# Kernel optimization log

Measured on AMD Instinct MI355X. Metric: run time of the kernel, lower is better.

Reference implementation:

```python
import jax, jax.numpy as jnp
import numpy as np

N_NODES = 100000
N_EDGES = 1600000
IN_C, HID_C, OUT_C = 128, 128, 64


def setup_inputs() -> dict:
    key = jax.random.key(0)
    ks = jax.random.split(key, 8)
    x = jax.random.normal(ks[0], (N_NODES, IN_C), dtype=jnp.float32)
    edge_index = jax.random.randint(ks[1], (2, N_EDGES), 0, N_NODES, dtype=jnp.int32)
    def lin(k, fan_in, fan_out):
        # kaiming-uniform-ish init like torch Linear
        bound = 1.0 / np.sqrt(fan_in)
        return jax.random.uniform(k, (fan_in, fan_out), dtype=jnp.float32, minval=-bound, maxval=bound)
    W1_l = lin(ks[2], IN_C, HID_C)
    W1_r = lin(ks[3], IN_C, HID_C)
    b1 = jnp.zeros((HID_C,), jnp.float32)
    W2_l = lin(ks[4], HID_C, OUT_C)
    W2_r = lin(ks[5], HID_C, OUT_C)
    b2 = jnp.zeros((OUT_C,), jnp.float32)
    return {"x": x, "edge_index": edge_index,
            "W1_l": W1_l, "W1_r": W1_r, "b1": b1,
            "W2_l": W2_l, "W2_r": W2_r, "b2": b2}


def _sage_conv(x, src, dst, W_l, W_r, b, n_nodes):
    # mean-aggregate neighbor features: gather x[src], scatter-add to dst, / degree
    msgs = jnp.take(x, src, axis=0)                       # [E, F]
    agg = jax.ops.segment_sum(msgs, dst, num_segments=n_nodes)  # [N, F]
    deg = jax.ops.segment_sum(jnp.ones((src.shape[0],), x.dtype), dst,
                              num_segments=n_nodes)       # [N]
    agg = agg / jnp.maximum(deg, 1.0)[:, None]
    return agg @ W_l + x @ W_r + b


def reference(x, edge_index, W1_l, W1_r, b1, W2_l, W2_r, b2):
    src, dst = edge_index[0], edge_index[1]
    n = x.shape[0]
    h = _sage_conv(x, src, dst, W1_l, W1_r, b1, n)
    h = jax.nn.relu(h)
    # dropout is identity in eval/inference mode
    out = _sage_conv(h, src, dst, W2_l, W2_r, b2, n)
    return out
```

## Files before the change

kernel.cpp:

```cpp
#include <hip/hip_runtime.h>

constexpr int NNODES = 100000;
constexpr int NEDGES = 1600000;
constexpr int K = 128;
constexpr int NBUCKET = 391;
constexpr int BCAP = 6144;
constexpr int A_EPB = NEDGES / 256;

typedef __attribute__((ext_vector_type(8))) short bf16x8;
typedef __attribute__((ext_vector_type(4))) float f32x4;

__device__ __forceinline__ unsigned short f2bf(float f) {
    unsigned u = __float_as_uint(f);
    unsigned r = (u + 0x7fffu + ((u >> 16) & 1u)) >> 16;
    return (unsigned short)r;
}
__device__ __forceinline__ void acc2(float& a0, float& a1, unsigned u) {
    a0 += __uint_as_float(u << 16);
    a1 += __uint_as_float(u & 0xffff0000u);
}
__device__ __forceinline__ void acc8(float* a, uint4 v) {
    acc2(a[0], a[1], v.x); acc2(a[2], a[3], v.y);
    acc2(a[4], a[5], v.z); acc2(a[6], a[7], v.w);
}

__global__ void zero_int_kernel(int* __restrict__ p, int n) {
    int i = blockIdx.x * 256 + threadIdx.x;
    if (i < n) p[i] = 0;
}

__global__ void xcast_kernel(const float4* __restrict__ in, uint4* __restrict__ out, int n8) {
    int i = blockIdx.x * 256 + threadIdx.x;
    if (i >= n8) return;
    float4 a = in[2 * i], b = in[2 * i + 1];
    uint4 w;
    w.x = (unsigned)f2bf(a.x) | ((unsigned)f2bf(a.y) << 16);
    w.y = (unsigned)f2bf(a.z) | ((unsigned)f2bf(a.w) << 16);
    w.z = (unsigned)f2bf(b.x) | ((unsigned)f2bf(b.y) << 16);
    w.w = (unsigned)f2bf(b.z) | ((unsigned)f2bf(b.w) << 16);
    out[i] = w;
}

__global__ void wprep_kernel(const float* __restrict__ W1l, const float* __restrict__ W1r,
                             const float* __restrict__ W2l, const float* __restrict__ W2r,
                             unsigned short* __restrict__ Wt1l, unsigned short* __restrict__ Wt1r,
                             unsigned short* __restrict__ Wt2) {
    int idx = blockIdx.x * 256 + threadIdx.x;
    if (idx >= 128 * 128) return;
    int n = idx >> 7, k = idx & 127;
    Wt1l[idx] = f2bf(W1l[k * 128 + n]);
    Wt1r[idx] = f2bf(W1r[k * 128 + n]);
    Wt2[idx]  = f2bf(n < 64 ? W2l[k * 64 + n] : W2r[k * 64 + (n - 64)]);
}

__global__ __launch_bounds__(256) void binA_kernel(
    const int* __restrict__ src, const int* __restrict__ dst,
    int* __restrict__ bucket_alloc, int2* __restrict__ regions)
{
    __shared__ int hist[NBUCKET];
    __shared__ int lstart[NBUCKET];
    __shared__ int gbase[NBUCKET];
    __shared__ int cur[NBUCKET];
    __shared__ int sD[A_EPB];
    __shared__ int sS[A_EPB];
    __shared__ int oD[A_EPB];
    __shared__ int oS[A_EPB];
    const int tid = threadIdx.x;
    for (int i = tid; i < NBUCKET; i += 256) hist[i] = 0;
    __syncthreads();
    const int e0 = blockIdx.x * A_EPB;
    for (int i = tid; i < A_EPB; i += 256) {
        int d = dst[e0 + i];
        sD[i] = d; sS[i] = src[e0 + i];
        atomicAdd(&hist[d >> 8], 1);
    }
    __syncthreads();
    if (tid == 0) {
        int acc = 0;
        for (int b = 0; b < NBUCKET; ++b) { lstart[b] = acc; acc += hist[b]; }
    }
    __syncthreads();
    for (int b = tid; b < NBUCKET; b += 256) {
        gbase[b] = atomicAdd(&bucket_alloc[b], hist[b]);
        cur[b] = lstart[b];
    }
    __syncthreads();
    for (int i = tid; i < A_EPB; i += 256) {
        int d = sD[i];
        int p = atomicAdd(&cur[d >> 8], 1);
        oD[p] = d; oS[p] = sS[i];
    }
    __syncthreads();
    for (int j = tid; j < A_EPB; j += 256) {
        int d = oD[j];
        int b = d >> 8;
        int pos = gbase[b] + (j - lstart[b]);
        if (pos < BCAP)
            regions[(size_t)b * BCAP + pos] = make_int2(d, oS[j]);
    }
}

__global__ void scanB_kernel(const int* __restrict__ bucket_alloc, int* __restrict__ bucket_base) {
    __shared__ int tmp[512];
    int t = threadIdx.x;
    int v = (t < NBUCKET) ? min(bucket_alloc[t], BCAP) : 0;
    tmp[t] = v;
    __syncthreads();
    #pragma unroll
    for (int off = 1; off < 512; off <<= 1) {
        int u = (t >= off) ? tmp[t - off] : 0;
        __syncthreads();
        tmp[t] += u;
        __syncthreads();
    }
    if (t < NBUCKET) bucket_base[t] = tmp[t] - v;
}

__global__ __launch_bounds__(256) void binB_kernel(
    const int2* __restrict__ regions, const int* __restrict__ bucket_alloc,
    const int* __restrict__ bucket_base,
    int* __restrict__ row_start, int* __restrict__ row_end, int* __restrict__ csr_src)
{
    __shared__ int hist[256];
    __shared__ int loff[256];
    __shared__ int cur[256];
    __shared__ int sD[BCAP];
    __shared__ int sS[BCAP];
    __shared__ int sorted[BCAP];
    const int b = blockIdx.x;
    const int tid = threadIdx.x;
    const int n = min(bucket_alloc[b], BCAP);
    const int base = bucket_base[b];
    hist[tid] = 0;
    __syncthreads();
    for (int i = tid; i < n; i += 256) {
        int2 rec = regions[(size_t)b * BCAP + i];
        sD[i] = rec.x; sS[i] = rec.y;
        atomicAdd(&hist[rec.x & 255], 1);
    }
    __syncthreads();
    int v = hist[tid];
    loff[tid] = v;
    __syncthreads();
    #pragma unroll
    for (int off = 1; off < 256; off <<= 1) {
        int u = (tid >= off) ? loff[tid - off] : 0;
        __syncthreads();
        loff[tid] += u;
        __syncthreads();
    }
    int excl = loff[tid] - v;
    cur[tid] = excl;
    int node = b * 256 + tid;
    if (node < NNODES) {
        row_start[node] = base + excl;
        row_end[node] = base + excl + v;
    }
    __syncthreads();
    for (int i = tid; i < n; i += 256) {
        int p = atomicAdd(&cur[sD[i] & 255], 1);
        sorted[p] = sS[i];
    }
    __syncthreads();
    for (int j = tid; j < n; j += 256)
        csr_src[base + j] = sorted[j];
}

__device__ __forceinline__ int xcd_swizzle(int bid, int nwg) {
    int xcd = bid & 7;
    int idx = bid >> 3;
    int q = nwg >> 3, r = nwg & 7;
    int base = (xcd < r) ? xcd * (q + 1) : r * (q + 1) + (xcd - r) * q;
    return base + idx;
}

template<int F, bool ADDV, bool OUTBF>
__global__ void gather_mean_bf16_kernel(const int* __restrict__ row_start,
                                        const int* __restrict__ row_end,
                                        const int* __restrict__ csr_src,
                                        const unsigned short* __restrict__ feat,
                                        const float* __restrict__ add,
                                        void* __restrict__ outp, int nwg) {
    constexpr int G = F / 8;
    constexpr int NPB = 256 / G;
    int blk = xcd_swizzle(blockIdx.x, nwg);
    int node = blk * NPB + threadIdx.x / G;
    int lane = threadIdx.x % G;
    if (node >= NNODES) return;
    int beg = row_start[node];
    int end = row_end[node];
    const uint4* fp = reinterpret_cast<const uint4*>(feat);
    float a[8];
    #pragma unroll
    for (int q = 0; q < 8; ++q) a[q] = 0.f;
    int j = beg;
    for (; j + 3 < end; j += 4) {
        int s0 = csr_src[j];
        int s1 = csr_src[j + 1];
        int s2 = csr_src[j + 2];
        int s3 = csr_src[j + 3];
        uint4 v0 = fp[(size_t)s0 * G + lane];
        uint4 v1 = fp[(size_t)s1 * G + lane];
        uint4 v2 = fp[(size_t)s2 * G + lane];
        uint4 v3 = fp[(size_t)s3 * G + lane];
        acc8(a, v0); acc8(a, v1); acc8(a, v2); acc8(a, v3);
    }
    for (; j < end; ++j) {
        uint4 v0 = fp[(size_t)csr_src[j] * G + lane];
        acc8(a, v0);
    }
    float inv = 1.0f / fmaxf((float)(end - beg), 1.0f);
    #pragma unroll
    for (int q = 0; q < 8; ++q) a[q] *= inv;
    if (OUTBF) {
        uint4 w;
        w.x = (unsigned)f2bf(a[0]) | ((unsigned)f2bf(a[1]) << 16);
        w.y = (unsigned)f2bf(a[2]) | ((unsigned)f2bf(a[3]) << 16);
        w.z = (unsigned)f2bf(a[4]) | ((unsigned)f2bf(a[5]) << 16);
        w.w = (unsigned)f2bf(a[6]) | ((unsigned)f2bf(a[7]) << 16);
        reinterpret_cast<uint4*>(outp)[(size_t)node * G + lane] = w;
    } else {
        float4 o0, o1;
        o0.x = a[0]; o0.y = a[1]; o0.z = a[2]; o0.w = a[3];
        o1.x = a[4]; o1.y = a[5]; o1.z = a[6]; o1.w = a[7];
        if (ADDV) {
            const float4* ap = reinterpret_cast<const float4*>(add + (size_t)node * F + lane * 8);
            float4 r0 = ap[0], r1 = ap[1];
            o0.x += r0.x; o0.y += r0.y; o0.z += r0.z; o0.w += r0.w;
            o1.x += r1.x; o1.y += r1.y; o1.z += r1.z; o1.w += r1.w;
        }
        float4* op = reinterpret_cast<float4*>((float*)outp + (size_t)node * F + lane * 8);
        op[0] = o0; op[1] = o1;
    }
}

template<bool LAYER2>
__global__ __launch_bounds__(256) void mfma_gemm_kernel(
    const unsigned short* __restrict__ A1, const unsigned short* __restrict__ A2,
    const unsigned short* __restrict__ Wt1, const unsigned short* __restrict__ Wt2,
    const float* __restrict__ bias,
    unsigned short* __restrict__ outB, float* __restrict__ outF, int M)
{
    const int wave = threadIdx.x >> 6;
    const int lane = threadIdx.x & 63;
    const int rsub = lane & 15;
    const int kgrp = lane >> 4;
    const int koff = kgrp * 8;
    const int row0 = blockIdx.x * 128 + wave * 32;
    const int ar0 = row0 + rsub;
    const int ar1 = row0 + 16 + rsub;
    const bool v0 = ar0 < M, v1 = ar1 < M;

    f32x4 acc[2][8];
    #pragma unroll
    for (int t = 0; t < 2; ++t)
        #pragma unroll
        for (int n = 0; n < 8; ++n) acc[t][n] = (f32x4){0.f, 0.f, 0.f, 0.f};

    #pragma unroll
    for (int mat = 0; mat < (LAYER2 ? 1 : 2); ++mat) {
        const unsigned short* __restrict__ A = mat ? A2 : A1;
        const unsigned short* __restrict__ W = mat ? Wt2 : Wt1;
        #pragma unroll
        for (int kk = 0; kk < 128; kk += 32) {
            bf16x8 a0 = {0, 0, 0, 0, 0, 0, 0, 0};
            bf16x8 a1 = {0, 0, 0, 0, 0, 0, 0, 0};
            if (v0) a0 = *reinterpret_cast<const bf16x8*>(A + (size_t)ar0 * 128 + kk + koff);
            if (v1) a1 = *reinterpret_cast<const bf16x8*>(A + (size_t)ar1 * 128 + kk + koff);
            #pragma unroll
            for (int n = 0; n < 8; ++n) {
                bf16x8 w = *reinterpret_cast<const bf16x8*>(W + (size_t)(n * 16 + rsub) * 128 + kk + koff);
                acc[0][n] = __builtin_amdgcn_mfma_f32_16x16x32_bf16(w, a0, acc[0][n], 0, 0, 0);
                acc[1][n] = __builtin_amdgcn_mfma_f32_16x16x32_bf16(w, a1, acc[1][n], 0, 0, 0);
            }
        }
    }

    if (!LAYER2) {
        float4 bv[8];
        #pragma unroll
        for (int n = 0; n < 8; ++n)
            bv[n] = *reinterpret_cast<const float4*>(bias + n * 16 + kgrp * 4);
        #pragma unroll
        for (int t = 0; t < 2; ++t) {
            int ar = t ? ar1 : ar0;
            if (!(t ? v1 : v0)) continue;
            #pragma unroll
            for (int n = 0; n < 8; ++n) {
                float e0 = fmaxf(acc[t][n][0] + bv[n].x, 0.f);
                float e1 = fmaxf(acc[t][n][1] + bv[n].y, 0.f);
                float e2 = fmaxf(acc[t][n][2] + bv[n].z, 0.f);
                float e3 = fmaxf(acc[t][n][3] + bv[n].w, 0.f);
                uint2 pw;
                pw.x = (unsigned)f2bf(e0) | ((unsigned)f2bf(e1) << 16);
                pw.y = (unsigned)f2bf(e2) | ((unsigned)f2bf(e3) << 16);
                *reinterpret_cast<uint2*>(outB + (size_t)ar * 128 + n * 16 + kgrp * 4) = pw;
            }
        }
    } else {
        float4 bv[4];
        #pragma unroll
        for (int n = 0; n < 4; ++n)
            bv[n] = *reinterpret_cast<const float4*>(bias + n * 16 + kgrp * 4);
        #pragma unroll
        for (int t = 0; t < 2; ++t) {
            int ar = t ? ar1 : ar0;
            if (!(t ? v1 : v0)) continue;
            #pragma unroll
            for (int n = 0; n < 4; ++n) {
                uint2 pw;
                pw.x = (unsigned)f2bf(acc[t][n][0]) | ((unsigned)f2bf(acc[t][n][1]) << 16);
                pw.y = (unsigned)f2bf(acc[t][n][2]) | ((unsigned)f2bf(acc[t][n][3]) << 16);
                *reinterpret_cast<uint2*>(outB + (size_t)ar * 64 + n * 16 + kgrp * 4) = pw;
            }
            #pragma unroll
            for (int n = 0; n < 4; ++n) {
                float4 o;
                o.x = acc[t][n + 4][0] + bv[n].x;
                o.y = acc[t][n + 4][1] + bv[n].y;
                o.z = acc[t][n + 4][2] + bv[n].z;
                o.w = acc[t][n + 4][3] + bv[n].w;
                *reinterpret_cast<float4*>(outF + (size_t)ar * 64 + n * 16 + kgrp * 4) = o;
            }
        }
    }
}

extern "C" void kernel_launch(void* const* d_in, const int* in_sizes, int n_in,
                              void* d_out, int out_size, void* d_ws, size_t ws_size,
                              hipStream_t stream)
{
    const float* x   = (const float*)d_in[0];
    const int*   ei  = (const int*)d_in[1];
    const float* W1l = (const float*)d_in[2];
    const float* W1r = (const float*)d_in[3];
    const float* b1  = (const float*)d_in[4];
    const float* W2l = (const float*)d_in[5];
    const float* W2r = (const float*)d_in[6];
    const float* b2  = (const float*)d_in[7];
    const int* src = ei;
    const int* dst = ei + NEDGES;

    char* ws = (char*)d_ws;
    int*   bucket_alloc = (int*)(ws + 0);
    int*   bucket_base  = (int*)(ws + 1664);
    int*   row_start = (int*)(ws + 400128);
    int*   row_end   = (int*)(ws + 800256);
    unsigned short* Wt1l = (unsigned short*)(ws + 1203712);
    unsigned short* Wt1r = (unsigned short*)(ws + 1236480);
    unsigned short* Wt2  = (unsigned short*)(ws + 1269248);
    int*   csr_src   = (int*)(ws + 1302016);
    unsigned short* agg1b = (unsigned short*)(ws + 7702016);
    unsigned short* p     = (unsigned short*)(ws + 7702016);
    float* r         = (float*)(ws + 20502016);
    int2*  regions   = (int2*)(ws + 20502016);
    unsigned short* h_bf16 = (unsigned short*)(ws + 46102016);
    unsigned short* x_bf16 = (unsigned short*)(ws + 71702016);
    float* out       = (float*)d_out;

    zero_int_kernel<<<2, 256, 0, stream>>>(bucket_alloc, NBUCKET);
    binA_kernel<<<256, 256, 0, stream>>>(src, dst, bucket_alloc, regions);
    xcast_kernel<<<(NNODES * K / 8 + 255) / 256, 256, 0, stream>>>(
        (const float4*)x, (uint4*)x_bf16, NNODES * K / 8);
    wprep_kernel<<<64, 256, 0, stream>>>(W1l, W1r, W2l, W2r, Wt1l, Wt1r, Wt2);
    scanB_kernel<<<1, 512, 0, stream>>>(bucket_alloc, bucket_base);
    binB_kernel<<<NBUCKET, 256, 0, stream>>>(regions, bucket_alloc, bucket_base,
                                             row_start, row_end, csr_src);

    {
        int nwg = (NNODES + 15) / 16;
        gather_mean_bf16_kernel<128, false, true><<<nwg, 256, 0, stream>>>(
            row_start, row_end, csr_src, x_bf16, nullptr, agg1b, nwg);
    }
    mfma_gemm_kernel<false><<<(NNODES + 127) / 128, 256, 0, stream>>>(
        agg1b, x_bf16, Wt1l, Wt1r, b1, h_bf16, nullptr, NNODES);

    mfma_gemm_kernel<true><<<(NNODES + 127) / 128, 256, 0, stream>>>(
        h_bf16, nullptr, Wt2, nullptr, b2, p, r, NNODES);
    {
        int nwg = (NNODES + 31) / 32;
        gather_mean_bf16_kernel<64, true, false><<<nwg, 256, 0, stream>>>(
            row_start, row_end, csr_src, p, r, out, nwg);
    }
}
```

Baseline: 230.8 us.

## Slice layer-1 bf16 features into 16-column slabs for cache-local gathers

Stores x (and the layer-1 aggregate) in a feature-sliced layout of eight 16-column slabs, each contiguous across all nodes. The layer-1 gather runs one slice per block, so each slice's working set (about 3.2MB) can stay in L2 during random neighbor reads. The GEMM reads A from the sliced layout with strided addressing. The risks are that csr_src and the row pointers are now read eight times, each gather load is only 16 bytes, and the GEMM A loads are less contiguous.

```diff
diff --git a/kernel.cpp b/kernel.cpp
--- a/kernel.cpp
+++ b/kernel.cpp
@@ -6,6 +6,8 @@
 constexpr int NBUCKET = 391;
 constexpr int BCAP = 6144;
 constexpr int A_EPB = NEDGES / 256;
+constexpr int NSL = 8;
+constexpr size_t SLSTRIDE = (size_t)NNODES * 16;
 
 typedef __attribute__((ext_vector_type(8))) short bf16x8;
 typedef __attribute__((ext_vector_type(4))) float f32x4;
@@ -29,16 +31,19 @@
     if (i < n) p[i] = 0;
 }
 
-__global__ void xcast_kernel(const float4* __restrict__ in, uint4* __restrict__ out, int n8) {
+__global__ void xcast_sliced_kernel(const float* __restrict__ x, unsigned short* __restrict__ x_sl) {
     int i = blockIdx.x * 256 + threadIdx.x;
-    if (i >= n8) return;
-    float4 a = in[2 * i], b = in[2 * i + 1];
+    if (i >= NNODES * 16) return;
+    int node = i >> 4, cg = i & 15;
+    const float4* src = reinterpret_cast<const float4*>(x + (size_t)node * 128 + cg * 8);
+    float4 a = src[0], b = src[1];
     uint4 w;
     w.x = (unsigned)f2bf(a.x) | ((unsigned)f2bf(a.y) << 16);
     w.y = (unsigned)f2bf(a.z) | ((unsigned)f2bf(a.w) << 16);
     w.z = (unsigned)f2bf(b.x) | ((unsigned)f2bf(b.y) << 16);
     w.w = (unsigned)f2bf(b.z) | ((unsigned)f2bf(b.w) << 16);
-    out[i] = w;
+    int s = cg >> 1, half = cg & 1;
+    reinterpret_cast<uint4*>(x_sl + s * SLSTRIDE)[(size_t)node * 2 + half] = w;
 }
 
 __global__ void wprep_kernel(const float* __restrict__ W1l, const float* __restrict__ W1r,
@@ -174,17 +179,54 @@
     return base + idx;
 }
 
-template<int F, bool ADDV, bool OUTBF>
+__global__ __launch_bounds__(256) void gather_mean_sliced_kernel(
+    const int* __restrict__ row_start, const int* __restrict__ row_end,
+    const int* __restrict__ csr_src, const unsigned short* __restrict__ feat_sl,
+    unsigned short* __restrict__ out_sl)
+{
+    int slice = blockIdx.x & 7;
+    int chunk = blockIdx.x >> 3;
+    int node = chunk * 128 + (threadIdx.x >> 1);
+    int half = threadIdx.x & 1;
+    if (node >= NNODES) return;
+    const uint4* fp = reinterpret_cast<const uint4*>(feat_sl + slice * SLSTRIDE);
+    int beg = row_start[node];
+    int end = row_end[node];
+    float a[8];
+    #pragma unroll
+    for (int q = 0; q < 8; ++q) a[q] = 0.f;
+    int j = beg;
+    for (; j + 3 < end; j += 4) {
+        int s0 = csr_src[j];
+        int s1 = csr_src[j + 1];
+        int s2 = csr_src[j + 2];
+        int s3 = csr_src[j + 3];
+        uint4 v0 = fp[(size_t)s0 * 2 + half];
+        uint4 v1 = fp[(size_t)s1 * 2 + half];
+        uint4 v2 = fp[(size_t)s2 * 2 + half];
+        uint4 v3 = fp[(size_t)s3 * 2 + half];
+        acc8(a, v0); acc8(a, v1); acc8(a, v2); acc8(a, v3);
+    }
+    for (; j < end; ++j)
+        acc8(a, fp[(size_t)csr_src[j] * 2 + half]);
+    float inv = 1.0f / fmaxf((float)(end - beg), 1.0f);
+    uint4 w;
+    w.x = (unsigned)f2bf(a[0] * inv) | ((unsigned)f2bf(a[1] * inv) << 16);
+    w.y = (unsigned)f2bf(a[2] * inv) | ((unsigned)f2bf(a[3] * inv) << 16);
+    w.z = (unsigned)f2bf(a[4] * inv) | ((unsigned)f2bf(a[5] * inv) << 16);
+    w.w = (unsigned)f2bf(a[6] * inv) | ((unsigned)f2bf(a[7] * inv) << 16);
+    reinterpret_cast<uint4*>(out_sl + slice * SLSTRIDE)[(size_t)node * 2 + half] = w;
+}
+
 __global__ void gather_mean_bf16_kernel(const int* __restrict__ row_start,
                                         const int* __restrict__ row_end,
                                         const int* __restrict__ csr_src,
                                         const unsigned short* __restrict__ feat,
                                         const float* __restrict__ add,
-                                        void* __restrict__ outp, int nwg) {
-    constexpr int G = F / 8;
-    constexpr int NPB = 256 / G;
+                                        float* __restrict__ outp, int nwg) {
+    constexpr int G = 8;
     int blk = xcd_swizzle(blockIdx.x, nwg);
-    int node = blk * NPB + threadIdx.x / G;
+    int node = blk * 32 + threadIdx.x / G;
     int lane = threadIdx.x % G;
     if (node >= NNODES) return;
     int beg = row_start[node];
@@ -205,36 +247,21 @@
         uint4 v3 = fp[(size_t)s3 * G + lane];
         acc8(a, v0); acc8(a, v1); acc8(a, v2); acc8(a, v3);
     }
-    for (; j < end; ++j) {
-        uint4 v0 = fp[(size_t)csr_src[j] * G + lane];
-        acc8(a, v0);
-    }
+    for (; j < end; ++j)
+        acc8(a, fp[(size_t)csr_src[j] * G + lane]);
     float inv = 1.0f / fmaxf((float)(end - beg), 1.0f);
-    #pragma unroll
-    for (int q = 0; q < 8; ++q) a[q] *= inv;
-    if (OUTBF) {
-        uint4 w;
-        w.x = (unsigned)f2bf(a[0]) | ((unsigned)f2bf(a[1]) << 16);
-        w.y = (unsigned)f2bf(a[2]) | ((unsigned)f2bf(a[3]) << 16);
-        w.z = (unsigned)f2bf(a[4]) | ((unsigned)f2bf(a[5]) << 16);
-        w.w = (unsigned)f2bf(a[6]) | ((unsigned)f2bf(a[7]) << 16);
-        reinterpret_cast<uint4*>(outp)[(size_t)node * G + lane] = w;
-    } else {
-        float4 o0, o1;
-        o0.x = a[0]; o0.y = a[1]; o0.z = a[2]; o0.w = a[3];
-        o1.x = a[4]; o1.y = a[5]; o1.z = a[6]; o1.w = a[7];
-        if (ADDV) {
-            const float4* ap = reinterpret_cast<const float4*>(add + (size_t)node * F + lane * 8);
-            float4 r0 = ap[0], r1 = ap[1];
-            o0.x += r0.x; o0.y += r0.y; o0.z += r0.z; o0.w += r0.w;
-            o1.x += r1.x; o1.y += r1.y; o1.z += r1.z; o1.w += r1.w;
-        }
-        float4* op = reinterpret_cast<float4*>((float*)outp + (size_t)node * F + lane * 8);
-        op[0] = o0; op[1] = o1;
-    }
-}
-
-template<bool LAYER2>
+    const float4* ap = reinterpret_cast<const float4*>(add + (size_t)node * 64 + lane * 8);
+    float4 r0 = ap[0], r1 = ap[1];
+    float4 o0, o1;
+    o0.x = a[0] * inv + r0.x; o0.y = a[1] * inv + r0.y;
+    o0.z = a[2] * inv + r0.z; o0.w = a[3] * inv + r0.w;
+    o1.x = a[4] * inv + r1.x; o1.y = a[5] * inv + r1.y;
+    o1.z = a[6] * inv + r1.z; o1.w = a[7] * inv + r1.w;
+    float4* op = reinterpret_cast<float4*>(outp + (size_t)node * 64 + lane * 8);
+    op[0] = o0; op[1] = o1;
+}
+
+template<bool LAYER2, bool SLICED>
 __global__ __launch_bounds__(256) void mfma_gemm_kernel(
     const unsigned short* __restrict__ A1, const unsigned short* __restrict__ A2,
     const unsigned short* __restrict__ Wt1, const unsigned short* __restrict__ Wt2,
@@ -265,8 +292,15 @@
         for (int kk = 0; kk < 128; kk += 32) {
             bf16x8 a0 = {0, 0, 0, 0, 0, 0, 0, 0};
             bf16x8 a1 = {0, 0, 0, 0, 0, 0, 0, 0};
-            if (v0) a0 = *reinterpret_cast<const bf16x8*>(A + (size_t)ar0 * 128 + kk + koff);
-            if (v1) a1 = *reinterpret_cast<const bf16x8*>(A + (size_t)ar1 * 128 + kk + koff);
+            if (SLICED) {
+                int k = kk + koff;
+                size_t off = (size_t)(k >> 4) * SLSTRIDE + (size_t)((k >> 3) & 1) * 8;
+                if (v0) a0 = *reinterpret_cast<const bf16x8*>(A + off + (size_t)ar0 * 16);
+                if (v1) a1 = *reinterpret_cast<const bf16x8*>(A + off + (size_t)ar1 * 16);
+            } else {
+                if (v0) a0 = *reinterpret_cast<const bf16x8*>(A + (size_t)ar0 * 128 + kk + koff);
+                if (v1) a1 = *reinterpret_cast<const bf16x8*>(A + (size_t)ar1 * 128 + kk + koff);
+            }
             #pragma unroll
             for (int n = 0; n < 8; ++n) {
                 bf16x8 w = *reinterpret_cast<const bf16x8*>(W + (size_t)(n * 16 + rsub) * 128 + kk + koff);
@@ -350,36 +384,32 @@
     unsigned short* Wt1r = (unsigned short*)(ws + 1236480);
     unsigned short* Wt2  = (unsigned short*)(ws + 1269248);
     int*   csr_src   = (int*)(ws + 1302016);
-    unsigned short* agg1b = (unsigned short*)(ws + 7702016);
-    unsigned short* p     = (unsigned short*)(ws + 7702016);
+    unsigned short* agg_sl = (unsigned short*)(ws + 7702016);
+    unsigned short* p      = (unsigned short*)(ws + 7702016);
     float* r         = (float*)(ws + 20502016);
     int2*  regions   = (int2*)(ws + 20502016);
     unsigned short* h_bf16 = (unsigned short*)(ws + 46102016);
-    unsigned short* x_bf16 = (unsigned short*)(ws + 71702016);
+    unsigned short* x_sl   = (unsigned short*)(ws + 71702016);
     float* out       = (float*)d_out;
 
     zero_int_kernel<<<2, 256, 0, stream>>>(bucket_alloc, NBUCKET);
     binA_kernel<<<256, 256, 0, stream>>>(src, dst, bucket_alloc, regions);
-    xcast_kernel<<<(NNODES * K / 8 + 255) / 256, 256, 0, stream>>>(
-        (const float4*)x, (uint4*)x_bf16, NNODES * K / 8);
+    xcast_sliced_kernel<<<(NNODES * 16 + 255) / 256, 256, 0, stream>>>(x, x_sl);
     wprep_kernel<<<64, 256, 0, stream>>>(W1l, W1r, W2l, W2r, Wt1l, Wt1r, Wt2);
     scanB_kernel<<<1, 512, 0, stream>>>(bucket_alloc, bucket_base);
     binB_kernel<<<NBUCKET, 256, 0, stream>>>(regions, bucket_alloc, bucket_base,
                                              row_start, row_end, csr_src);
 
-    {
-        int nwg = (NNODES + 15) / 16;
-        gather_mean_bf16_kernel<128, false, true><<<nwg, 256, 0, stream>>>(
-            row_start, row_end, csr_src, x_bf16, nullptr, agg1b, nwg);
-    }
-    mfma_gemm_kernel<false><<<(NNODES + 127) / 128, 256, 0, stream>>>(
-        agg1b, x_bf16, Wt1l, Wt1r, b1, h_bf16, nullptr, NNODES);
-
-    mfma_gemm_kernel<true><<<(NNODES + 127) / 128, 256, 0, stream>>>(
+    gather_mean_sliced_kernel<<<NSL * ((NNODES + 127) / 128), 256, 0, stream>>>(
+        row_start, row_end, csr_src, x_sl, agg_sl);
+    mfma_gemm_kernel<false, true><<<(NNODES + 127) / 128, 256, 0, stream>>>(
+        agg_sl, x_sl, Wt1l, Wt1r, b1, h_bf16, nullptr, NNODES);
+
+    mfma_gemm_kernel<true, false><<<(NNODES + 127) / 128, 256, 0, stream>>>(
         h_bf16, nullptr, Wt2, nullptr, b2, p, r, NNODES);
     {
         int nwg = (NNODES + 31) / 32;
-        gather_mean_bf16_kernel<64, true, false><<<nwg, 256, 0, stream>>>(
+        gather_mean_bf16_kernel<<<nwg, 256, 0, stream>>>(
             row_start, row_end, csr_src, p, r, out, nwg);
     }
 }
```

Result: slower. 257.7 us (+11.6%).
